# Kernel tuning notes

Hardware: AMD Instinct MI355X
Metric: run time of the kernel (lower is better)

## Reference

```python
import jax, jax.numpy as jnp
import numpy as np

H = 1024  # hidden_dim


def setup_inputs() -> dict:
    key = jax.random.key(0)
    ks = jax.random.split(key, 8)
    B, S = 32, 2048
    value = jax.random.normal(ks[0], (B, S, 2 * H), dtype=jnp.float32)
    query = jax.random.normal(ks[1], (B, 2 * H), dtype=jnp.float32)
    padding_mask = jnp.zeros((B, S), dtype=bool)
    pre_coverage = jax.random.uniform(ks[2], (B, S), dtype=jnp.float32)
    sc = 1.0 / np.sqrt(2 * H)
    Wv = jax.random.normal(ks[3], (2 * H, H), dtype=jnp.float32) * sc  # value_layer.weight^T
    Wq = jax.random.normal(ks[4], (2 * H, H), dtype=jnp.float32) * sc  # query_layer.weight^T
    We = jax.random.normal(ks[5], (H,), dtype=jnp.float32) * (1.0 / np.sqrt(H))  # energy_layer
    Wc = jax.random.normal(ks[6], (H,), dtype=jnp.float32)  # coverage_layer (Linear(1,H))
    return {"value": value, "query": query, "padding_mask": padding_mask,
            "pre_coverage": pre_coverage, "Wv": Wv, "Wq": Wq, "We": We, "Wc": Wc}


def reference(value, query, padding_mask, pre_coverage, Wv, Wq, We, Wc):
    # value: [B,S,2H], query: [B,2H], padding_mask: [B,S] bool, pre_coverage: [B,S]
    v = jnp.einsum('bsf,fh->bsh', value, Wv)          # projected values [B,S,H]
    q = (query @ Wq)[:, None, :]                       # [B,1,H]
    feat = q + v + pre_coverage[:, :, None] * Wc       # coverage term: Linear(1,H)
    scores = jnp.tanh(feat) @ We                       # [B,S]
    scores = jnp.where(padding_mask, -jnp.inf, scores)
    alphas = jax.nn.softmax(scores, axis=-1)           # [B,S]
    context = jnp.einsum('bs,bsh->bh', alphas, v)[:, None, :]  # [B,1,H]
    new_coverage = pre_coverage + alphas
    return context, alphas, new_coverage
```

## Files before the change

kernel.cpp:

```cpp
#include <hip/hip_runtime.h>
#include <hip/hip_bf16.h>

#define HD 1024
#define K2 2048
#define BATCH 32
#define SEQ 2048
#define M_TOT (BATCH * SEQ)

typedef __attribute__((ext_vector_type(4))) float f32x4;
typedef __attribute__((ext_vector_type(8))) short bf16x8;
typedef __attribute__((ext_vector_type(4))) unsigned short u16x4;
typedef __attribute__((ext_vector_type(8))) unsigned short u16x8;
typedef __attribute__((ext_vector_type(4))) unsigned int u32x4;

__device__ __forceinline__ float bf2f(unsigned short u) {
    unsigned int x = ((unsigned int)u) << 16;
    return __builtin_bit_cast(float, x);
}
__device__ __forceinline__ unsigned short f2bf(float f) {
    unsigned int x = __builtin_bit_cast(unsigned int, f);
    unsigned int lsb = (x >> 16) & 1u;
    x += 0x7fffu + lsb;
    return (unsigned short)(x >> 16);
}
__device__ __forceinline__ unsigned int cvt_pk(float lo, float hi) {
    unsigned int r;
    asm("v_cvt_pk_bf16_f32 %0, %1, %2" : "=v"(r) : "v"(lo), "v"(hi));
    return r;
}

__device__ __forceinline__ void load_lds_16B(const void* g, void* lds) {
    __builtin_amdgcn_global_load_lds(
        (const __attribute__((address_space(1))) unsigned int*)g,
        (__attribute__((address_space(3))) unsigned int*)lds,
        16, 0, 0);
}

__global__ __launch_bounds__(256) void wv_transpose_kernel(
        const float* __restrict__ Wv, unsigned short* __restrict__ WvT) {
    __shared__ float t[64][65];
    int n0 = blockIdx.x * 64;
    int k0 = blockIdx.y * 64;
    int tx = threadIdx.x & 63, ty = threadIdx.x >> 6;
#pragma unroll
    for (int rr = 0; rr < 16; ++rr) {
        int row = ty + rr * 4;
        t[row][tx] = Wv[(size_t)(k0 + row) * HD + n0 + tx];
    }
    __syncthreads();
#pragma unroll
    for (int rr = 0; rr < 16; ++rr) {
        int row = ty + rr * 4;
        WvT[(size_t)(n0 + row) * K2 + k0 + tx] = f2bf(t[tx][row]);
    }
}

__global__ __launch_bounds__(256) void qproj_kernel(
        const float* __restrict__ query, const float* __restrict__ Wq,
        float* __restrict__ qp) {
    int b = blockIdx.x >> 2;
    int h = ((blockIdx.x & 3) << 8) + threadIdx.x;
    const float* q = query + (size_t)b * K2;
    float acc = 0.f;
    for (int f = 0; f < K2; f += 4) {
        f32x4 qv = *reinterpret_cast<const f32x4*>(q + f);
        acc += qv.x * Wq[(size_t)f * HD + h];
        acc += qv.y * Wq[(size_t)(f + 1) * HD + h];
        acc += qv.z * Wq[(size_t)(f + 2) * HD + h];
        acc += qv.w * Wq[(size_t)(f + 3) * HD + h];
    }
    qp[b * HD + h] = acc;
}

#define NT 32

__device__ __forceinline__ f32x4 mfma_bf16(bf16x8 a, bf16x8 b, f32x4 c) {
    return __builtin_amdgcn_mfma_f32_16x16x32_bf16(a, b, c, 0, 0, 0);
}

template<int MB, int NB>
__device__ __forceinline__ void mfma_quad(f32x4 (&acc)[8][4],
        const bf16x8 (&af)[4][2], const bf16x8 (&bfv)[2][2]) {
#pragma unroll
    for (int f = 0; f < 4; ++f)
#pragma unroll
        for (int j = 0; j < 2; ++j) {
            acc[MB + f][NB + j] = mfma_bf16(af[f][0], bfv[j][0], acc[MB + f][NB + j]);
            acc[MB + f][NB + j] = mfma_bf16(af[f][1], bfv[j][1], acc[MB + f][NB + j]);
        }
}

__global__ __launch_bounds__(512, 2) void gemm8_kernel(
        const float* __restrict__ A,
        const unsigned short* __restrict__ BT,
        unsigned short* __restrict__ Vout) {
    __shared__ __align__(16) char lds[131072];

    const int tid  = threadIdx.x;
    const int lane = tid & 63;
    const int wave = tid >> 6;
    const int wr   = wave >> 2;
    const int wc   = wave & 3;

    int id  = blockIdx.x;
    int xcd = id & 7, sdx = id >> 3;
    int m0 = ((xcd << 5) | (sdx >> 2)) * 256;
    int n0 = (sdx & 3) * 256;

    const int off0   = wave * 1024 + lane * 16;
    const int srow   = off0 >> 7;
    const int chunk  = (off0 >> 4) & 7;
    const int schunk = chunk ^ (srow & 7);
    const unsigned short* Bs0 = BT + ((size_t)n0 + srow) * K2 + schunk * 8;
    const float* aBase = A + ((size_t)m0 + srow) * K2 + chunk * 8;
    const int woff = srow * 128 + schunk * 16;

    const int l15 = lane & 15, l4v = lane >> 4;
    const int kch0 = (l4v ^ (lane & 7)) << 4;
    const int kch1 = ((4 | l4v) ^ (lane & 7)) << 4;
    const int aRow = (wr * 128 + l15) * 128;
    const int bRow = (wc * 64 + l15) * 128;

    f32x4 acc[8][4] = {};

    f32x4 a0lo, a0hi, a1lo, a1hi, a2lo, a2hi, a3lo, a3hi;

#define LOAD_A(t_) do {                                                       \
        const float* _ap = aBase + (size_t)(t_) * 64;                         \
        a0lo = *(const f32x4*)(_ap);                                          \
        a0hi = *(const f32x4*)(_ap + 4);                                      \
        a1lo = *(const f32x4*)(_ap + (size_t)128 * K2);                       \
        a1hi = *(const f32x4*)(_ap + (size_t)128 * K2 + 4);                   \
        a2lo = *(const f32x4*)(_ap + (size_t)64 * K2);                        \
        a2hi = *(const f32x4*)(_ap + (size_t)64 * K2 + 4);                    \
        a3lo = *(const f32x4*)(_ap + (size_t)192 * K2);                       \
        a3hi = *(const f32x4*)(_ap + (size_t)192 * K2 + 4);                   \
    } while (0)

#define WRITE_A_P0(buf_) do {                                                 \
        u32x4 w0, w1;                                                         \
        w0.x = cvt_pk(a0lo.x, a0lo.y); w0.y = cvt_pk(a0lo.z, a0lo.w);         \
        w0.z = cvt_pk(a0hi.x, a0hi.y); w0.w = cvt_pk(a0hi.z, a0hi.w);         \
        w1.x = cvt_pk(a1lo.x, a1lo.y); w1.y = cvt_pk(a1lo.z, a1lo.w);         \
        w1.z = cvt_pk(a1hi.x, a1hi.y); w1.w = cvt_pk(a1hi.z, a1hi.w);         \
        *reinterpret_cast<u32x4*>(lds + (buf_) * 32768 + 0     + woff) = w0;  \
        *reinterpret_cast<u32x4*>(lds + (buf_) * 32768 + 16384 + woff) = w1;  \
    } while (0)

#define WRITE_A_P1(buf_) do {                                                 \
        u32x4 w2, w3;                                                         \
        w2.x = cvt_pk(a2lo.x, a2lo.y); w2.y = cvt_pk(a2lo.z, a2lo.w);         \
        w2.z = cvt_pk(a2hi.x, a2hi.y); w2.w = cvt_pk(a2hi.z, a2hi.w);         \
        w3.x = cvt_pk(a3lo.x, a3lo.y); w3.y = cvt_pk(a3lo.z, a3lo.w);         \
        w3.z = cvt_pk(a3hi.x, a3hi.y); w3.w = cvt_pk(a3hi.z, a3hi.w);         \
        *reinterpret_cast<u32x4*>(lds + (buf_) * 32768 + 8192  + woff) = w2;  \
        *reinterpret_cast<u32x4*>(lds + (buf_) * 32768 + 24576 + woff) = w3;  \
    } while (0)

#define STG_B(t_, h_, p_, buf_) \
    load_lds_16B(Bs0 + ((size_t)((h_) * 128 + (p_) * 64)) * K2 + (t_) * 64, \
                 lds + 65536 + (buf_) * 32768 + (h_) * 16384 + (p_) * 8192 + off0)

    LOAD_A(0);
    STG_B(0, 0, 0, 0); STG_B(0, 0, 1, 0); STG_B(0, 1, 0, 0); STG_B(0, 1, 1, 0);
    WRITE_A_P0(0); WRITE_A_P1(0);
    LOAD_A(1);
    STG_B(1, 0, 0, 1); STG_B(1, 0, 1, 1); STG_B(1, 1, 0, 1); STG_B(1, 1, 1, 1);
    WRITE_A_P0(1); WRITE_A_P1(1);
    asm volatile("s_waitcnt vmcnt(0) lgkmcnt(0)" ::: "memory");
    __builtin_amdgcn_s_barrier();

    bf16x8 afr[4][2], bf0[2][2], bf1[2][2];

    for (int t = 0; t < NT; ++t) {
        const int cur = t & 1;
        const char* La = lds + cur * 32768;
        const char* Lb = lds + 65536 + cur * 32768;
        const bool pf = (t + 2 < NT);

#pragma unroll
        for (int f = 0; f < 4; ++f) {
            afr[f][0] = *(const bf16x8*)(La + aRow + f * 2048 + kch0);
            afr[f][1] = *(const bf16x8*)(La + aRow + f * 2048 + kch1);
        }
#pragma unroll
        for (int j = 0; j < 2; ++j) {
            bf0[j][0] = *(const bf16x8*)(Lb + bRow + j * 2048 + kch0);
            bf0[j][1] = *(const bf16x8*)(Lb + bRow + j * 2048 + kch1);
        }
        if (pf) LOAD_A(t + 2);
        __builtin_amdgcn_s_barrier();
        asm volatile("s_waitcnt lgkmcnt(0)" ::: "memory");
        __builtin_amdgcn_s_setprio(1);
        mfma_quad<0, 0>(acc, afr, bf0);
        __builtin_amdgcn_s_setprio(0);
        __builtin_amdgcn_s_barrier();

#pragma unroll
        for (int j = 0; j < 2; ++j) {
            bf1[j][0] = *(const bf16x8*)(Lb + bRow + (2 + j) * 2048 + kch0);
            bf1[j][1] = *(const bf16x8*)(Lb + bRow + (2 + j) * 2048 + kch1);
        }
        __builtin_amdgcn_s_barrier();
        asm volatile("s_waitcnt lgkmcnt(0)" ::: "memory");
        __builtin_amdgcn_s_setprio(1);
        mfma_quad<0, 2>(acc, afr, bf1);
        __builtin_amdgcn_s_setprio(0);
        __builtin_amdgcn_s_barrier();

#pragma unroll
        for (int f = 0; f < 4; ++f) {
            afr[f][0] = *(const bf16x8*)(La + aRow + 8192 + f * 2048 + kch0);
            afr[f][1] = *(const bf16x8*)(La + aRow + 8192 + f * 2048 + kch1);
        }
        if (pf) {
            WRITE_A_P0(cur);
            STG_B(t + 2, 0, 0, cur); STG_B(t + 2, 0, 1, cur);
            STG_B(t + 2, 1, 0, cur); STG_B(t + 2, 1, 1, cur);
        }
        __builtin_amdgcn_s_barrier();
        asm volatile("s_waitcnt lgkmcnt(0)" ::: "memory");
        __builtin_amdgcn_s_setprio(1);
        mfma_quad<4, 2>(acc, afr, bf1);
        __builtin_amdgcn_s_setprio(0);
        __builtin_amdgcn_s_barrier();

        if (pf) WRITE_A_P1(cur);
        __builtin_amdgcn_s_barrier();
        asm volatile("s_waitcnt lgkmcnt(0)" ::: "memory");
        __builtin_amdgcn_s_setprio(1);
        mfma_quad<4, 0>(acc, afr, bf0);
        __builtin_amdgcn_s_setprio(0);
        if (t == NT - 2) asm volatile("s_waitcnt vmcnt(0)" ::: "memory");
        if (t < NT - 1) __builtin_amdgcn_s_barrier();
    }
#undef LOAD_A
#undef WRITE_A_P0
#undef WRITE_A_P1
#undef STG_B

#pragma unroll
    for (int fi = 0; fi < 8; ++fi) {
#pragma unroll
        for (int fj = 0; fj < 4; ++fj) {
            int row = m0 + wr * 128 + fi * 16 + l4v * 4;
            int col = n0 + wc * 64 + fj * 16 + l15;
#pragma unroll
            for (int r = 0; r < 4; ++r)
                Vout[(size_t)(row + r) * HD + col] = f2bf(acc[fi][fj][r]);
        }
    }
}

#define BM 128
#define BN 128
#define BK 32
__device__ __forceinline__ void swizzle_mn(int id, int& m0, int& n0) {
    int xcd = id & 7;
    int s = id >> 3;
    int m_idx = (xcd << 6) | (s >> 3);
    int n_idx = s & 7;
    m0 = m_idx * BM;
    n0 = n_idx * BN;
}

__global__ __launch_bounds__(256) void gemm_v_kernel(
        const float* __restrict__ A,
        const unsigned short* __restrict__ BT,
        unsigned short* __restrict__ Vout) {
    __shared__ __align__(16) unsigned short As[BM * BK];
    __shared__ __align__(16) unsigned short Bs[BN * BK];
    const int tid = threadIdx.x;
    const int lane = tid & 63;
    const int wave = tid >> 6;
    const int wr = wave >> 1, wc = wave & 1;
    int m0, n0;
    swizzle_mn(blockIdx.x, m0, n0);
    const int l15 = lane & 15;
    const int l4 = lane >> 4;

    f32x4 acc[4][4] = {};

    for (int kk = 0; kk < K2; kk += BK) {
#pragma unroll
        for (int i = 0; i < 4; ++i) {
            int c = i * 256 + tid;
            int row = c >> 3;
            int col = (c & 7) * 4;
            f32x4 v = *reinterpret_cast<const f32x4*>(
                A + (size_t)(m0 + row) * K2 + kk + col);
            u16x4 bv;
            bv.x = f2bf(v.x); bv.y = f2bf(v.y);
            bv.z = f2bf(v.z); bv.w = f2bf(v.w);
            *reinterpret_cast<u16x4*>(&As[row * BK + col]) = bv;
        }
#pragma unroll
        for (int i = 0; i < 2; ++i) {
            int cb = i * 256 + tid;
            int row = cb >> 2, col = (cb & 3) * 8;
            load_lds_16B(BT + (size_t)(n0 + row) * K2 + kk + col, ((char*)Bs) + cb * 16);
        }
        __syncthreads();

        bf16x8 af[4], bfr[4];
#pragma unroll
        for (int i = 0; i < 4; ++i) {
            int row = wr * 64 + i * 16 + l15;
            af[i] = *reinterpret_cast<const bf16x8*>(&As[row * BK + l4 * 8]);
        }
#pragma unroll
        for (int j = 0; j < 4; ++j) {
            int row = wc * 64 + j * 16 + l15;
            bfr[j] = *reinterpret_cast<const bf16x8*>(&Bs[row * BK + l4 * 8]);
        }
#pragma unroll
        for (int i = 0; i < 4; ++i)
#pragma unroll
            for (int j = 0; j < 4; ++j)
                acc[i][j] = __builtin_amdgcn_mfma_f32_16x16x32_bf16(
                    af[i], bfr[j], acc[i][j], 0, 0, 0);
        __syncthreads();
    }

#pragma unroll
    for (int i = 0; i < 4; ++i) {
#pragma unroll
        for (int j = 0; j < 4; ++j) {
            int row = m0 + wr * 64 + i * 16 + l4 * 4;
            int col = n0 + wc * 64 + j * 16 + l15;
#pragma unroll
            for (int r = 0; r < 4; ++r)
                Vout[(size_t)(row + r) * HD + col] = f2bf(acc[i][j][r]);
        }
    }
}

__global__ __launch_bounds__(256) void score_kernel(
        const unsigned short* __restrict__ V, const float* __restrict__ qp,
        const float* __restrict__ Wc, const float* __restrict__ We,
        const float* __restrict__ pre_cov, float* __restrict__ scores) {
    int lane = threadIdx.x & 63;
    int wave = threadIdx.x >> 6;
    int m = blockIdx.x * 4 + wave;
    int b = m >> 11;
    float pc = pre_cov[m];
    const unsigned short* vp = V + (size_t)m * HD;
    const float* qpb = qp + b * HD;
    float partial = 0.f;
#pragma unroll
    for (int e = 0; e < 16; ++e) {
        int h = e * 64 + lane;
        float f = bf2f(vp[h]) + qpb[h] + pc * Wc[h];
        float t = 1.f - 2.f / (__expf(2.f * f) + 1.f);
        partial += t * We[h];
    }
#pragma unroll
    for (int off = 32; off; off >>= 1)
        partial += __shfl_xor(partial, off);
    if (lane == 0) scores[m] = partial;
}

__global__ __launch_bounds__(256) void softmax_kernel(
        const float* __restrict__ scores, const unsigned char* __restrict__ mask,
        const float* __restrict__ pre_cov, float* __restrict__ out) {
    __shared__ float red[8];
    int b = blockIdx.x;
    int tid = threadIdx.x;
    int lane = tid & 63, wave = tid >> 6;
    float s[8];
#pragma unroll
    for (int i = 0; i < 8; ++i) {
        int idx = b * SEQ + i * 256 + tid;
        float v = scores[idx];
        if (mask[idx]) v = -INFINITY;
        s[i] = v;
    }
    float mx = s[0];
#pragma unroll
    for (int i = 1; i < 8; ++i) mx = fmaxf(mx, s[i]);
#pragma unroll
    for (int off = 32; off; off >>= 1) mx = fmaxf(mx, __shfl_xor(mx, off));
    if (lane == 0) red[wave] = mx;
    __syncthreads();
    mx = fmaxf(fmaxf(red[0], red[1]), fmaxf(red[2], red[3]));

    float e[8]; float sum = 0.f;
#pragma unroll
    for (int i = 0; i < 8; ++i) { e[i] = __expf(s[i] - mx); sum += e[i]; }
#pragma unroll
    for (int off = 32; off; off >>= 1) sum += __shfl_xor(sum, off);
    if (lane == 0) red[4 + wave] = sum;
    __syncthreads();
    sum = red[4] + red[5] + red[6] + red[7];
    float inv = 1.f / sum;
#pragma unroll
    for (int i = 0; i < 8; ++i) {
        int idx = b * SEQ + i * 256 + tid;
        float a = e[i] * inv;
        out[32768 + idx] = a;
        out[32768 + 65536 + idx] = pre_cov[idx] + a;
    }
}

__global__ __launch_bounds__(256) void ctx_part_kernel(
        const unsigned short* __restrict__ V, const float* __restrict__ out,
        float* __restrict__ part) {
    int blk = blockIdx.x;
    int sc = blk & 15;
    int b  = blk >> 4;
    int h4 = threadIdx.x * 4;
    const float* al = out + 32768 + b * SEQ + sc * 128;
    const unsigned short* vp = V + ((size_t)(b * SEQ + sc * 128)) * HD + h4;
    f32x4 acc = {};
#pragma unroll 4
    for (int s = 0; s < 128; ++s) {
        float a = al[s];
        u16x4 v = *reinterpret_cast<const u16x4*>(vp + (size_t)s * HD);
        acc.x += a * bf2f(v.x);
        acc.y += a * bf2f(v.y);
        acc.z += a * bf2f(v.z);
        acc.w += a * bf2f(v.w);
    }
    *reinterpret_cast<f32x4*>(&part[(size_t)(b * 16 + sc) * HD + h4]) = acc;
}

__global__ __launch_bounds__(256) void ctx_reduce_kernel(
        const float* __restrict__ part, float* __restrict__ out) {
    int idx = blockIdx.x * 256 + threadIdx.x;
    int b = idx >> 10, h = idx & 1023;
    float acc = 0.f;
#pragma unroll
    for (int sc = 0; sc < 16; ++sc)
        acc += part[(size_t)(b * 16 + sc) * HD + h];
    out[idx] = acc;
}

extern "C" void kernel_launch(void* const* d_in, const int* in_sizes, int n_in,
                              void* d_out, int out_size, void* d_ws, size_t ws_size,
                              hipStream_t stream) {
    const float* value          = (const float*)d_in[0];
    const float* query          = (const float*)d_in[1];
    const unsigned char* mask   = (const unsigned char*)d_in[2];
    const float* pre_cov        = (const float*)d_in[3];
    const float* Wv             = (const float*)d_in[4];
    const float* Wq             = (const float*)d_in[5];
    const float* We             = (const float*)d_in[6];
    const float* Wc             = (const float*)d_in[7];
    float* out = (float*)d_out;

    char* ws = (char*)d_ws;
    unsigned short* WvT = (unsigned short*)(ws);
    unsigned short* Vbf = (unsigned short*)(ws + ((size_t)4 << 20));
    float* qp           = (float*)(ws + ((size_t)132 << 20));
    float* scores       = (float*)(ws + ((size_t)132 << 20) + (128 << 10));
    float* part         = (float*)(ws + ((size_t)132 << 20) + (384 << 10));

    const bool bigws = ws_size >= ((size_t)136 << 20);

    hipLaunchKernelGGL(wv_transpose_kernel, dim3(16, 32), dim3(256), 0, stream, Wv, WvT);
    hipLaunchKernelGGL(qproj_kernel, dim3(128), dim3(256), 0, stream, query, Wq, qp);
    if (bigws) {
        hipLaunchKernelGGL(gemm8_kernel, dim3(1024), dim3(512), 0, stream, value, WvT, Vbf);
    } else {
        hipLaunchKernelGGL(gemm_v_kernel, dim3(4096), dim3(256), 0, stream, value, WvT, Vbf);
    }
    hipLaunchKernelGGL(score_kernel, dim3(M_TOT / 4), dim3(256), 0, stream,
                       Vbf, qp, Wc, We, pre_cov, scores);
    hipLaunchKernelGGL(softmax_kernel, dim3(BATCH), dim3(256), 0, stream,
                       scores, mask, pre_cov, out);
    hipLaunchKernelGGL(ctx_part_kernel, dim3(512), dim3(256), 0, stream, Vbf, out, part);
    hipLaunchKernelGGL(ctx_reduce_kernel, dim3(128), dim3(256), 0, stream, part, out);
}
```

Baseline: 504.0 us.

## Deepen A-tile global prefetch to three stages with ping-pong register sets

The fp32 A-operand global loads are now issued three K-steps ahead instead of two, using two alternating register sets (setA/setB) and a 2x manually unrolled main loop. The prologue issues the third load and waits only on older vmcnt, so global latency for A has more time to hide behind MFMA work. This doubles the register footprint for staged A data (32 more VGPRs), which under launch_bounds(512,2) risks spills or reduced scheduling freedom. The vmcnt(0) wait at t==NT-2 remains, and the inner loops lost their unroll pragmas inside the macro.

```diff
diff --git a/kernel.cpp b/kernel.cpp
--- a/kernel.cpp
+++ b/kernel.cpp
@@ -90,6 +90,40 @@
         }
 }
 
+struct ASet { f32x4 v0, v1, v2, v3, v4, v5, v6, v7; };
+
+__device__ __forceinline__ void load_a_set(const float* aBase, int t, ASet& s) {
+    const float* ap = aBase + (size_t)t * 64;
+    s.v0 = *(const f32x4*)(ap);
+    s.v1 = *(const f32x4*)(ap + 4);
+    s.v2 = *(const f32x4*)(ap + (size_t)128 * K2);
+    s.v3 = *(const f32x4*)(ap + (size_t)128 * K2 + 4);
+    s.v4 = *(const f32x4*)(ap + (size_t)64 * K2);
+    s.v5 = *(const f32x4*)(ap + (size_t)64 * K2 + 4);
+    s.v6 = *(const f32x4*)(ap + (size_t)192 * K2);
+    s.v7 = *(const f32x4*)(ap + (size_t)192 * K2 + 4);
+}
+
+__device__ __forceinline__ void write_a_p0(char* lds, int buf, int woff, const ASet& s) {
+    u32x4 w0, w1;
+    w0.x = cvt_pk(s.v0.x, s.v0.y); w0.y = cvt_pk(s.v0.z, s.v0.w);
+    w0.z = cvt_pk(s.v1.x, s.v1.y); w0.w = cvt_pk(s.v1.z, s.v1.w);
+    w1.x = cvt_pk(s.v2.x, s.v2.y); w1.y = cvt_pk(s.v2.z, s.v2.w);
+    w1.z = cvt_pk(s.v3.x, s.v3.y); w1.w = cvt_pk(s.v3.z, s.v3.w);
+    *reinterpret_cast<u32x4*>(lds + buf * 32768 + 0     + woff) = w0;
+    *reinterpret_cast<u32x4*>(lds + buf * 32768 + 16384 + woff) = w1;
+}
+
+__device__ __forceinline__ void write_a_p1(char* lds, int buf, int woff, const ASet& s) {
+    u32x4 w2, w3;
+    w2.x = cvt_pk(s.v4.x, s.v4.y); w2.y = cvt_pk(s.v4.z, s.v4.w);
+    w2.z = cvt_pk(s.v5.x, s.v5.y); w2.w = cvt_pk(s.v5.z, s.v5.w);
+    w3.x = cvt_pk(s.v6.x, s.v6.y); w3.y = cvt_pk(s.v6.z, s.v6.w);
+    w3.z = cvt_pk(s.v7.x, s.v7.y); w3.w = cvt_pk(s.v7.z, s.v7.w);
+    *reinterpret_cast<u32x4*>(lds + buf * 32768 + 8192  + woff) = w2;
+    *reinterpret_cast<u32x4*>(lds + buf * 32768 + 24576 + woff) = w3;
+}
+
 __global__ __launch_bounds__(512, 2) void gemm8_kernel(
         const float* __restrict__ A,
         const unsigned short* __restrict__ BT,
@@ -123,120 +157,88 @@
 
     f32x4 acc[8][4] = {};
 
-    f32x4 a0lo, a0hi, a1lo, a1hi, a2lo, a2hi, a3lo, a3hi;
-
-#define LOAD_A(t_) do {                                                       \
-        const float* _ap = aBase + (size_t)(t_) * 64;                         \
-        a0lo = *(const f32x4*)(_ap);                                          \
-        a0hi = *(const f32x4*)(_ap + 4);                                      \
-        a1lo = *(const f32x4*)(_ap + (size_t)128 * K2);                       \
-        a1hi = *(const f32x4*)(_ap + (size_t)128 * K2 + 4);                   \
-        a2lo = *(const f32x4*)(_ap + (size_t)64 * K2);                        \
-        a2hi = *(const f32x4*)(_ap + (size_t)64 * K2 + 4);                    \
-        a3lo = *(const f32x4*)(_ap + (size_t)192 * K2);                       \
-        a3hi = *(const f32x4*)(_ap + (size_t)192 * K2 + 4);                   \
-    } while (0)
-
-#define WRITE_A_P0(buf_) do {                                                 \
-        u32x4 w0, w1;                                                         \
-        w0.x = cvt_pk(a0lo.x, a0lo.y); w0.y = cvt_pk(a0lo.z, a0lo.w);         \
-        w0.z = cvt_pk(a0hi.x, a0hi.y); w0.w = cvt_pk(a0hi.z, a0hi.w);         \
-        w1.x = cvt_pk(a1lo.x, a1lo.y); w1.y = cvt_pk(a1lo.z, a1lo.w);         \
-        w1.z = cvt_pk(a1hi.x, a1hi.y); w1.w = cvt_pk(a1hi.z, a1hi.w);         \
-        *reinterpret_cast<u32x4*>(lds + (buf_) * 32768 + 0     + woff) = w0;  \
-        *reinterpret_cast<u32x4*>(lds + (buf_) * 32768 + 16384 + woff) = w1;  \
-    } while (0)
-
-#define WRITE_A_P1(buf_) do {                                                 \
-        u32x4 w2, w3;                                                         \
-        w2.x = cvt_pk(a2lo.x, a2lo.y); w2.y = cvt_pk(a2lo.z, a2lo.w);         \
-        w2.z = cvt_pk(a2hi.x, a2hi.y); w2.w = cvt_pk(a2hi.z, a2hi.w);         \
-        w3.x = cvt_pk(a3lo.x, a3lo.y); w3.y = cvt_pk(a3lo.z, a3lo.w);         \
-        w3.z = cvt_pk(a3hi.x, a3hi.y); w3.w = cvt_pk(a3hi.z, a3hi.w);         \
-        *reinterpret_cast<u32x4*>(lds + (buf_) * 32768 + 8192  + woff) = w2;  \
-        *reinterpret_cast<u32x4*>(lds + (buf_) * 32768 + 24576 + woff) = w3;  \
-    } while (0)
+    ASet setA, setB;
 
 #define STG_B(t_, h_, p_, buf_) \
     load_lds_16B(Bs0 + ((size_t)((h_) * 128 + (p_) * 64)) * K2 + (t_) * 64, \
                  lds + 65536 + (buf_) * 32768 + (h_) * 16384 + (p_) * 8192 + off0)
 
-    LOAD_A(0);
+    load_a_set(aBase, 0, setA);
     STG_B(0, 0, 0, 0); STG_B(0, 0, 1, 0); STG_B(0, 1, 0, 0); STG_B(0, 1, 1, 0);
-    WRITE_A_P0(0); WRITE_A_P1(0);
-    LOAD_A(1);
+    write_a_p0(lds, 0, woff, setA); write_a_p1(lds, 0, woff, setA);
+    load_a_set(aBase, 1, setA);
     STG_B(1, 0, 0, 1); STG_B(1, 0, 1, 1); STG_B(1, 1, 0, 1); STG_B(1, 1, 1, 1);
-    WRITE_A_P0(1); WRITE_A_P1(1);
-    asm volatile("s_waitcnt vmcnt(0) lgkmcnt(0)" ::: "memory");
+    write_a_p0(lds, 1, woff, setA); write_a_p1(lds, 1, woff, setA);
+    load_a_set(aBase, 2, setA);
+    asm volatile("s_waitcnt vmcnt(8) lgkmcnt(0)" ::: "memory");
     __builtin_amdgcn_s_barrier();
 
     bf16x8 afr[4][2], bf0[2][2], bf1[2][2];
 
-    for (int t = 0; t < NT; ++t) {
-        const int cur = t & 1;
-        const char* La = lds + cur * 32768;
-        const char* Lb = lds + 65536 + cur * 32768;
-        const bool pf = (t + 2 < NT);
-
-#pragma unroll
-        for (int f = 0; f < 4; ++f) {
-            afr[f][0] = *(const bf16x8*)(La + aRow + f * 2048 + kch0);
-            afr[f][1] = *(const bf16x8*)(La + aRow + f * 2048 + kch1);
-        }
-#pragma unroll
-        for (int j = 0; j < 2; ++j) {
-            bf0[j][0] = *(const bf16x8*)(Lb + bRow + j * 2048 + kch0);
-            bf0[j][1] = *(const bf16x8*)(Lb + bRow + j * 2048 + kch1);
-        }
-        if (pf) LOAD_A(t + 2);
-        __builtin_amdgcn_s_barrier();
-        asm volatile("s_waitcnt lgkmcnt(0)" ::: "memory");
-        __builtin_amdgcn_s_setprio(1);
-        mfma_quad<0, 0>(acc, afr, bf0);
-        __builtin_amdgcn_s_setprio(0);
-        __builtin_amdgcn_s_barrier();
-
-#pragma unroll
-        for (int j = 0; j < 2; ++j) {
-            bf1[j][0] = *(const bf16x8*)(Lb + bRow + (2 + j) * 2048 + kch0);
-            bf1[j][1] = *(const bf16x8*)(Lb + bRow + (2 + j) * 2048 + kch1);
-        }
-        __builtin_amdgcn_s_barrier();
-        asm volatile("s_waitcnt lgkmcnt(0)" ::: "memory");
-        __builtin_amdgcn_s_setprio(1);
-        mfma_quad<0, 2>(acc, afr, bf1);
-        __builtin_amdgcn_s_setprio(0);
-        __builtin_amdgcn_s_barrier();
-
-#pragma unroll
-        for (int f = 0; f < 4; ++f) {
-            afr[f][0] = *(const bf16x8*)(La + aRow + 8192 + f * 2048 + kch0);
-            afr[f][1] = *(const bf16x8*)(La + aRow + 8192 + f * 2048 + kch1);
-        }
-        if (pf) {
-            WRITE_A_P0(cur);
-            STG_B(t + 2, 0, 0, cur); STG_B(t + 2, 0, 1, cur);
-            STG_B(t + 2, 1, 0, cur); STG_B(t + 2, 1, 1, cur);
-        }
-        __builtin_amdgcn_s_barrier();
-        asm volatile("s_waitcnt lgkmcnt(0)" ::: "memory");
-        __builtin_amdgcn_s_setprio(1);
-        mfma_quad<4, 2>(acc, afr, bf1);
-        __builtin_amdgcn_s_setprio(0);
-        __builtin_amdgcn_s_barrier();
-
-        if (pf) WRITE_A_P1(cur);
-        __builtin_amdgcn_s_barrier();
-        asm volatile("s_waitcnt lgkmcnt(0)" ::: "memory");
-        __builtin_amdgcn_s_setprio(1);
-        mfma_quad<4, 0>(acc, afr, bf0);
-        __builtin_amdgcn_s_setprio(0);
-        if (t == NT - 2) asm volatile("s_waitcnt vmcnt(0)" ::: "memory");
-        if (t < NT - 1) __builtin_amdgcn_s_barrier();
-    }
-#undef LOAD_A
-#undef WRITE_A_P0
-#undef WRITE_A_P1
+#define ITER(t_, CUR, NXT) do {                                               \
+        const int cur = (t_) & 1;                                             \
+        const char* La = lds + cur * 32768;                                   \
+        const char* Lb = lds + 65536 + cur * 32768;                           \
+        const bool pf = ((t_) + 2 < NT);                                      \
+          \
+        for (int f = 0; f < 4; ++f) {                                         \
+            afr[f][0] = *(const bf16x8*)(La + aRow + f * 2048 + kch0);        \
+            afr[f][1] = *(const bf16x8*)(La + aRow + f * 2048 + kch1);        \
+        }                                                                     \
+        for (int j = 0; j < 2; ++j) {                                         \
+            bf0[j][0] = *(const bf16x8*)(Lb + bRow + j * 2048 + kch0);        \
+            bf0[j][1] = *(const bf16x8*)(Lb + bRow + j * 2048 + kch1);        \
+        }                                                                     \
+        if ((t_) + 3 < NT) load_a_set(aBase, (t_) + 3, NXT);                  \
+        __builtin_amdgcn_s_barrier();                                         \
+        asm volatile("s_waitcnt lgkmcnt(0)" ::: "memory");                    \
+        __builtin_amdgcn_s_setprio(1);                                        \
+        mfma_quad<0, 0>(acc, afr, bf0);                                       \
+        __builtin_amdgcn_s_setprio(0);                                        \
+        __builtin_amdgcn_s_barrier();                                         \
+                                          \
+        for (int j = 0; j < 2; ++j) {                                         \
+            bf1[j][0] = *(const bf16x8*)(Lb + bRow + (2 + j) * 2048 + kch0);  \
+            bf1[j][1] = *(const bf16x8*)(Lb + bRow + (2 + j) * 2048 + kch1);  \
+        }                                                                     \
+        __builtin_amdgcn_s_barrier();                                         \
+        asm volatile("s_waitcnt lgkmcnt(0)" ::: "memory");                    \
+        __builtin_amdgcn_s_setprio(1);                                        \
+        mfma_quad<0, 2>(acc, afr, bf1);                                       \
+        __builtin_amdgcn_s_setprio(0);                                        \
+        __builtin_amdgcn_s_barrier();                                         \
+         \
+        for (int f = 0; f < 4; ++f) {                                         \
+            afr[f][0] = *(const bf16x8*)(La + aRow + 8192 + f * 2048 + kch0); \
+            afr[f][1] = *(const bf16x8*)(La + aRow + 8192 + f * 2048 + kch1); \
+        }                                                                     \
+        if (pf) {                                                             \
+            write_a_p0(lds, cur, woff, CUR);                                  \
+            STG_B((t_) + 2, 0, 0, cur); STG_B((t_) + 2, 0, 1, cur);           \
+            STG_B((t_) + 2, 1, 0, cur); STG_B((t_) + 2, 1, 1, cur);           \
+        }                                                                     \
+        __builtin_amdgcn_s_barrier();                                         \
+        asm volatile("s_waitcnt lgkmcnt(0)" ::: "memory");                    \
+        __builtin_amdgcn_s_setprio(1);                                        \
+        mfma_quad<4, 2>(acc, afr, bf1);                                       \
+        __builtin_amdgcn_s_setprio(0);                                        \
+        __builtin_amdgcn_s_barrier();                                         \
+                         \
+        if (pf) write_a_p1(lds, cur, woff, CUR);                              \
+        __builtin_amdgcn_s_barrier();                                         \
+        asm volatile("s_waitcnt lgkmcnt(0)" ::: "memory");                    \
+        __builtin_amdgcn_s_setprio(1);                                        \
+        mfma_quad<4, 0>(acc, afr, bf0);                                       \
+        __builtin_amdgcn_s_setprio(0);                                        \
+        if ((t_) == NT - 2) asm volatile("s_waitcnt vmcnt(0)" ::: "memory");  \
+        if ((t_) < NT - 1) __builtin_amdgcn_s_barrier();                      \
+    } while (0)
+
+    for (int t = 0; t < NT; t += 2) {
+        ITER(t, setA, setB);
+        ITER(t + 1, setB, setA);
+    }
+#undef ITER
 #undef STG_B
 
 #pragma unroll
```

Result: slower. 939.7 us (+86.5%).

## Replace 256x256 8-wave GEMM with 128x128 4-wave tile kernel

Applied to the files above, without the earlier changes.

Swaps the 256x256-tile, 512-thread value-projection GEMM for a 128x128-tile, 256-thread variant with half the LDS. A-tile global loads, conversion and LDS writes are regrouped into one set per stage, and the first three K-steps are prefetched. The aim is more resident blocks per CU and finer-grained scheduling in exchange for lower per-tile data reuse, so the fp32 A matrix and the B matrix are fetched from global memory more times overall.

```diff
diff --git a/kernel.cpp b/kernel.cpp
--- a/kernel.cpp
+++ b/kernel.cpp
@@ -79,10 +79,10 @@
 }
 
 template<int MB, int NB>
-__device__ __forceinline__ void mfma_quad(f32x4 (&acc)[8][4],
-        const bf16x8 (&af)[4][2], const bf16x8 (&bfv)[2][2]) {
-#pragma unroll
-    for (int f = 0; f < 4; ++f)
+__device__ __forceinline__ void mfma_q4(f32x4 (&acc)[4][4],
+        const bf16x8 (&af)[2][2], const bf16x8 (&bfv)[2][2]) {
+#pragma unroll
+    for (int f = 0; f < 2; ++f)
 #pragma unroll
         for (int j = 0; j < 2; ++j) {
             acc[MB + f][NB + j] = mfma_bf16(af[f][0], bfv[j][0], acc[MB + f][NB + j]);
@@ -90,26 +90,56 @@
         }
 }
 
-__global__ __launch_bounds__(512, 2) void gemm8_kernel(
+struct ASet { f32x4 v0, v1, v2, v3, v4, v5, v6, v7; };
+
+__device__ __forceinline__ void load_a_set(const float* aBase, int t, ASet& s) {
+    const float* ap = aBase + (size_t)t * 64;
+    s.v0 = *(const f32x4*)(ap);
+    s.v1 = *(const f32x4*)(ap + 4);
+    s.v2 = *(const f32x4*)(ap + (size_t)32 * K2);
+    s.v3 = *(const f32x4*)(ap + (size_t)32 * K2 + 4);
+    s.v4 = *(const f32x4*)(ap + (size_t)64 * K2);
+    s.v5 = *(const f32x4*)(ap + (size_t)64 * K2 + 4);
+    s.v6 = *(const f32x4*)(ap + (size_t)96 * K2);
+    s.v7 = *(const f32x4*)(ap + (size_t)96 * K2 + 4);
+}
+
+__device__ __forceinline__ void write_a(char* lds, int buf, int woff, const ASet& s) {
+    u32x4 w0, w1, w2, w3;
+    w0.x = cvt_pk(s.v0.x, s.v0.y); w0.y = cvt_pk(s.v0.z, s.v0.w);
+    w0.z = cvt_pk(s.v1.x, s.v1.y); w0.w = cvt_pk(s.v1.z, s.v1.w);
+    w1.x = cvt_pk(s.v2.x, s.v2.y); w1.y = cvt_pk(s.v2.z, s.v2.w);
+    w1.z = cvt_pk(s.v3.x, s.v3.y); w1.w = cvt_pk(s.v3.z, s.v3.w);
+    w2.x = cvt_pk(s.v4.x, s.v4.y); w2.y = cvt_pk(s.v4.z, s.v4.w);
+    w2.z = cvt_pk(s.v5.x, s.v5.y); w2.w = cvt_pk(s.v5.z, s.v5.w);
+    w3.x = cvt_pk(s.v6.x, s.v6.y); w3.y = cvt_pk(s.v6.z, s.v6.w);
+    w3.z = cvt_pk(s.v7.x, s.v7.y); w3.w = cvt_pk(s.v7.z, s.v7.w);
+    *reinterpret_cast<u32x4*>(lds + buf * 16384 + 0     + woff) = w0;
+    *reinterpret_cast<u32x4*>(lds + buf * 16384 + 4096  + woff) = w1;
+    *reinterpret_cast<u32x4*>(lds + buf * 16384 + 8192  + woff) = w2;
+    *reinterpret_cast<u32x4*>(lds + buf * 16384 + 12288 + woff) = w3;
+}
+
+__global__ __launch_bounds__(256, 2) void gemm128f_kernel(
         const float* __restrict__ A,
         const unsigned short* __restrict__ BT,
         unsigned short* __restrict__ Vout) {
-    __shared__ __align__(16) char lds[131072];
+    __shared__ __align__(16) char lds[65536];
 
     const int tid  = threadIdx.x;
     const int lane = tid & 63;
     const int wave = tid >> 6;
-    const int wr   = wave >> 2;
-    const int wc   = wave & 3;
+    const int wr   = wave >> 1;
+    const int wc   = wave & 1;
 
     int id  = blockIdx.x;
     int xcd = id & 7, sdx = id >> 3;
-    int m0 = ((xcd << 5) | (sdx >> 2)) * 256;
-    int n0 = (sdx & 3) * 256;
-
-    const int off0   = wave * 1024 + lane * 16;
-    const int srow   = off0 >> 7;
-    const int chunk  = (off0 >> 4) & 7;
+    int m0 = ((xcd << 6) | (sdx >> 3)) * 128;
+    int n0 = (sdx & 7) * 128;
+
+    const int off0   = tid * 16;
+    const int srow   = tid >> 3;
+    const int chunk  = tid & 7;
     const int schunk = chunk ^ (srow & 7);
     const unsigned short* Bs0 = BT + ((size_t)n0 + srow) * K2 + schunk * 8;
     const float* aBase = A + ((size_t)m0 + srow) * K2 + chunk * 8;
@@ -118,68 +148,36 @@
     const int l15 = lane & 15, l4v = lane >> 4;
     const int kch0 = (l4v ^ (lane & 7)) << 4;
     const int kch1 = ((4 | l4v) ^ (lane & 7)) << 4;
-    const int aRow = (wr * 128 + l15) * 128;
+    const int aRow = (wr * 64 + l15) * 128;
     const int bRow = (wc * 64 + l15) * 128;
 
-    f32x4 acc[8][4] = {};
-
-    f32x4 a0lo, a0hi, a1lo, a1hi, a2lo, a2hi, a3lo, a3hi;
-
-#define LOAD_A(t_) do {                                                       \
-        const float* _ap = aBase + (size_t)(t_) * 64;                         \
-        a0lo = *(const f32x4*)(_ap);                                          \
-        a0hi = *(const f32x4*)(_ap + 4);                                      \
-        a1lo = *(const f32x4*)(_ap + (size_t)128 * K2);                       \
-        a1hi = *(const f32x4*)(_ap + (size_t)128 * K2 + 4);                   \
-        a2lo = *(const f32x4*)(_ap + (size_t)64 * K2);                        \
-        a2hi = *(const f32x4*)(_ap + (size_t)64 * K2 + 4);                    \
-        a3lo = *(const f32x4*)(_ap + (size_t)192 * K2);                       \
-        a3hi = *(const f32x4*)(_ap + (size_t)192 * K2 + 4);                   \
-    } while (0)
-
-#define WRITE_A_P0(buf_) do {                                                 \
-        u32x4 w0, w1;                                                         \
-        w0.x = cvt_pk(a0lo.x, a0lo.y); w0.y = cvt_pk(a0lo.z, a0lo.w);         \
-        w0.z = cvt_pk(a0hi.x, a0hi.y); w0.w = cvt_pk(a0hi.z, a0hi.w);         \
-        w1.x = cvt_pk(a1lo.x, a1lo.y); w1.y = cvt_pk(a1lo.z, a1lo.w);         \
-        w1.z = cvt_pk(a1hi.x, a1hi.y); w1.w = cvt_pk(a1hi.z, a1hi.w);         \
-        *reinterpret_cast<u32x4*>(lds + (buf_) * 32768 + 0     + woff) = w0;  \
-        *reinterpret_cast<u32x4*>(lds + (buf_) * 32768 + 16384 + woff) = w1;  \
-    } while (0)
-
-#define WRITE_A_P1(buf_) do {                                                 \
-        u32x4 w2, w3;                                                         \
-        w2.x = cvt_pk(a2lo.x, a2lo.y); w2.y = cvt_pk(a2lo.z, a2lo.w);         \
-        w2.z = cvt_pk(a2hi.x, a2hi.y); w2.w = cvt_pk(a2hi.z, a2hi.w);         \
-        w3.x = cvt_pk(a3lo.x, a3lo.y); w3.y = cvt_pk(a3lo.z, a3lo.w);         \
-        w3.z = cvt_pk(a3hi.x, a3hi.y); w3.w = cvt_pk(a3hi.z, a3hi.w);         \
-        *reinterpret_cast<u32x4*>(lds + (buf_) * 32768 + 8192  + woff) = w2;  \
-        *reinterpret_cast<u32x4*>(lds + (buf_) * 32768 + 24576 + woff) = w3;  \
-    } while (0)
-
-#define STG_B(t_, h_, p_, buf_) \
-    load_lds_16B(Bs0 + ((size_t)((h_) * 128 + (p_) * 64)) * K2 + (t_) * 64, \
-                 lds + 65536 + (buf_) * 32768 + (h_) * 16384 + (p_) * 8192 + off0)
-
-    LOAD_A(0);
-    STG_B(0, 0, 0, 0); STG_B(0, 0, 1, 0); STG_B(0, 1, 0, 0); STG_B(0, 1, 1, 0);
-    WRITE_A_P0(0); WRITE_A_P1(0);
-    LOAD_A(1);
-    STG_B(1, 0, 0, 1); STG_B(1, 0, 1, 1); STG_B(1, 1, 0, 1); STG_B(1, 1, 1, 1);
-    WRITE_A_P0(1); WRITE_A_P1(1);
-    asm volatile("s_waitcnt vmcnt(0) lgkmcnt(0)" ::: "memory");
+    f32x4 acc[4][4] = {};
+    ASet s;
+
+#define STG_B(t_, p_, buf_) \
+    load_lds_16B(Bs0 + ((size_t)(32 * (p_))) * K2 + (t_) * 64, \
+                 lds + 32768 + (buf_) * 16384 + (p_) * 4096 + off0)
+
+    load_a_set(aBase, 0, s);
+    STG_B(0, 0, 0); STG_B(0, 1, 0); STG_B(0, 2, 0); STG_B(0, 3, 0);
+    write_a(lds, 0, woff, s);
+    load_a_set(aBase, 1, s);
+    STG_B(1, 0, 1); STG_B(1, 1, 1); STG_B(1, 2, 1); STG_B(1, 3, 1);
+    write_a(lds, 1, woff, s);
+    load_a_set(aBase, 2, s);
+    asm volatile("s_waitcnt lgkmcnt(0)" ::: "memory");
     __builtin_amdgcn_s_barrier();
 
-    bf16x8 afr[4][2], bf0[2][2], bf1[2][2];
+    bf16x8 afr[2][2], bf0[2][2], bf1[2][2];
 
     for (int t = 0; t < NT; ++t) {
         const int cur = t & 1;
-        const char* La = lds + cur * 32768;
-        const char* Lb = lds + 65536 + cur * 32768;
+        const char* La = lds + cur * 16384;
+        const char* Lb = lds + 32768 + cur * 16384;
         const bool pf = (t + 2 < NT);
 
 #pragma unroll
-        for (int f = 0; f < 4; ++f) {
+        for (int f = 0; f < 2; ++f) {
             afr[f][0] = *(const bf16x8*)(La + aRow + f * 2048 + kch0);
             afr[f][1] = *(const bf16x8*)(La + aRow + f * 2048 + kch1);
         }
@@ -188,11 +186,11 @@
             bf0[j][0] = *(const bf16x8*)(Lb + bRow + j * 2048 + kch0);
             bf0[j][1] = *(const bf16x8*)(Lb + bRow + j * 2048 + kch1);
         }
-        if (pf) LOAD_A(t + 2);
+        if (pf) load_a_set(aBase, t + 2, s);
         __builtin_amdgcn_s_barrier();
         asm volatile("s_waitcnt lgkmcnt(0)" ::: "memory");
         __builtin_amdgcn_s_setprio(1);
-        mfma_quad<0, 0>(acc, afr, bf0);
+        mfma_q4<0, 0>(acc, afr, bf0);
         __builtin_amdgcn_s_setprio(0);
         __builtin_amdgcn_s_barrier();
 
@@ -204,46 +202,40 @@
         __builtin_amdgcn_s_barrier();
         asm volatile("s_waitcnt lgkmcnt(0)" ::: "memory");
         __builtin_amdgcn_s_setprio(1);
-        mfma_quad<0, 2>(acc, afr, bf1);
+        mfma_q4<0, 2>(acc, afr, bf1);
         __builtin_amdgcn_s_setprio(0);
         __builtin_amdgcn_s_barrier();
 
 #pragma unroll
-        for (int f = 0; f < 4; ++f) {
-            afr[f][0] = *(const bf16x8*)(La + aRow + 8192 + f * 2048 + kch0);
-            afr[f][1] = *(const bf16x8*)(La + aRow + 8192 + f * 2048 + kch1);
-        }
-        if (pf) {
-            WRITE_A_P0(cur);
-            STG_B(t + 2, 0, 0, cur); STG_B(t + 2, 0, 1, cur);
-            STG_B(t + 2, 1, 0, cur); STG_B(t + 2, 1, 1, cur);
-        }
+        for (int f = 0; f < 2; ++f) {
+            afr[f][0] = *(const bf16x8*)(La + aRow + 4096 + f * 2048 + kch0);
+            afr[f][1] = *(const bf16x8*)(La + aRow + 4096 + f * 2048 + kch1);
+        }
+        if (pf) { STG_B(t + 2, 0, cur); STG_B(t + 2, 1, cur);
+                  STG_B(t + 2, 2, cur); STG_B(t + 2, 3, cur); }
         __builtin_amdgcn_s_barrier();
         asm volatile("s_waitcnt lgkmcnt(0)" ::: "memory");
         __builtin_amdgcn_s_setprio(1);
-        mfma_quad<4, 2>(acc, afr, bf1);
+        mfma_q4<2, 2>(acc, afr, bf1);
         __builtin_amdgcn_s_setprio(0);
         __builtin_amdgcn_s_barrier();
 
-        if (pf) WRITE_A_P1(cur);
+        if (pf) write_a(lds, cur, woff, s);
         __builtin_amdgcn_s_barrier();
         asm volatile("s_waitcnt lgkmcnt(0)" ::: "memory");
         __builtin_amdgcn_s_setprio(1);
-        mfma_quad<4, 0>(acc, afr, bf0);
+        mfma_q4<2, 0>(acc, afr, bf0);
         __builtin_amdgcn_s_setprio(0);
         if (t == NT - 2) asm volatile("s_waitcnt vmcnt(0)" ::: "memory");
         if (t < NT - 1) __builtin_amdgcn_s_barrier();
     }
-#undef LOAD_A
-#undef WRITE_A_P0
-#undef WRITE_A_P1
 #undef STG_B
 
 #pragma unroll
-    for (int fi = 0; fi < 8; ++fi) {
+    for (int fi = 0; fi < 4; ++fi) {
 #pragma unroll
         for (int fj = 0; fj < 4; ++fj) {
-            int row = m0 + wr * 128 + fi * 16 + l4v * 4;
+            int row = m0 + wr * 64 + fi * 16 + l4v * 4;
             int col = n0 + wc * 64 + fj * 16 + l15;
 #pragma unroll
             for (int r = 0; r < 4; ++r)
@@ -460,7 +452,7 @@
     hipLaunchKernelGGL(wv_transpose_kernel, dim3(16, 32), dim3(256), 0, stream, Wv, WvT);
     hipLaunchKernelGGL(qproj_kernel, dim3(128), dim3(256), 0, stream, query, Wq, qp);
     if (bigws) {
-        hipLaunchKernelGGL(gemm8_kernel, dim3(1024), dim3(512), 0, stream, value, WvT, Vbf);
+        hipLaunchKernelGGL(gemm128f_kernel, dim3(4096), dim3(256), 0, stream, value, WvT, Vbf);
     } else {
         hipLaunchKernelGGL(gemm_v_kernel, dim3(4096), dim3(256), 0, stream, value, WvT, Vbf);
     }
```

Measured after the change: 590.0 us. +17.1%, slower.

## Fuse tanh-energy score computation into GEMM epilogue with partial-score reduction

Applied to the files above, without the earlier changes.

Computes the tanh(q+v+cov*Wc)·We score contributions directly from the fp32 GEMM accumulators in the gemm8 epilogue. Each wave writes a per-row partial over its 64 columns into a 16-wide partial buffer, and a new softmax kernel sums those partials. This removes the separate score kernel, which re-read the full bf16 V matrix. It adds epilogue ALU work, shuffles and extra partial-score traffic, and needs a larger workspace threshold for the fast path.

```diff
diff --git a/kernel.cpp b/kernel.cpp
--- a/kernel.cpp
+++ b/kernel.cpp
@@ -93,7 +93,12 @@
 __global__ __launch_bounds__(512, 2) void gemm8_kernel(
         const float* __restrict__ A,
         const unsigned short* __restrict__ BT,
-        unsigned short* __restrict__ Vout) {
+        unsigned short* __restrict__ Vout,
+        const float* __restrict__ qp,
+        const float* __restrict__ Wc,
+        const float* __restrict__ We,
+        const float* __restrict__ pre_cov,
+        float* __restrict__ scores_part) {
     __shared__ __align__(16) char lds[131072];
 
     const int tid  = threadIdx.x;
@@ -137,36 +142,40 @@
         a3hi = *(const f32x4*)(_ap + (size_t)192 * K2 + 4);                   \
     } while (0)
 
-#define WRITE_A_P0(buf_) do {                                                 \
+#define WRITE_A_P0() do {                                                     \
         u32x4 w0, w1;                                                         \
         w0.x = cvt_pk(a0lo.x, a0lo.y); w0.y = cvt_pk(a0lo.z, a0lo.w);         \
         w0.z = cvt_pk(a0hi.x, a0hi.y); w0.w = cvt_pk(a0hi.z, a0hi.w);         \
         w1.x = cvt_pk(a1lo.x, a1lo.y); w1.y = cvt_pk(a1lo.z, a1lo.w);         \
         w1.z = cvt_pk(a1hi.x, a1hi.y); w1.w = cvt_pk(a1hi.z, a1hi.w);         \
-        *reinterpret_cast<u32x4*>(lds + (buf_) * 32768 + 0     + woff) = w0;  \
-        *reinterpret_cast<u32x4*>(lds + (buf_) * 32768 + 16384 + woff) = w1;  \
+        *reinterpret_cast<u32x4*>(lds + _buf * 32768 + 0     + woff) = w0;    \
+        *reinterpret_cast<u32x4*>(lds + _buf * 32768 + 16384 + woff) = w1;    \
     } while (0)
 
-#define WRITE_A_P1(buf_) do {                                                 \
+#define WRITE_A_P1() do {                                                     \
         u32x4 w2, w3;                                                         \
         w2.x = cvt_pk(a2lo.x, a2lo.y); w2.y = cvt_pk(a2lo.z, a2lo.w);         \
         w2.z = cvt_pk(a2hi.x, a2hi.y); w2.w = cvt_pk(a2hi.z, a2hi.w);         \
         w3.x = cvt_pk(a3lo.x, a3lo.y); w3.y = cvt_pk(a3lo.z, a3lo.w);         \
         w3.z = cvt_pk(a3hi.x, a3hi.y); w3.w = cvt_pk(a3hi.z, a3hi.w);         \
-        *reinterpret_cast<u32x4*>(lds + (buf_) * 32768 + 8192  + woff) = w2;  \
-        *reinterpret_cast<u32x4*>(lds + (buf_) * 32768 + 24576 + woff) = w3;  \
+        *reinterpret_cast<u32x4*>(lds + _buf * 32768 + 8192  + woff) = w2;    \
+        *reinterpret_cast<u32x4*>(lds + _buf * 32768 + 24576 + woff) = w3;    \
     } while (0)
 
 #define STG_B(t_, h_, p_, buf_) \
     load_lds_16B(Bs0 + ((size_t)((h_) * 128 + (p_) * 64)) * K2 + (t_) * 64, \
                  lds + 65536 + (buf_) * 32768 + (h_) * 16384 + (p_) * 8192 + off0)
 
-    LOAD_A(0);
-    STG_B(0, 0, 0, 0); STG_B(0, 0, 1, 0); STG_B(0, 1, 0, 0); STG_B(0, 1, 1, 0);
-    WRITE_A_P0(0); WRITE_A_P1(0);
-    LOAD_A(1);
-    STG_B(1, 0, 0, 1); STG_B(1, 0, 1, 1); STG_B(1, 1, 0, 1); STG_B(1, 1, 1, 1);
-    WRITE_A_P0(1); WRITE_A_P1(1);
+    {
+        int _buf = 0;
+        LOAD_A(0);
+        STG_B(0, 0, 0, 0); STG_B(0, 0, 1, 0); STG_B(0, 1, 0, 0); STG_B(0, 1, 1, 0);
+        WRITE_A_P0(); WRITE_A_P1();
+        _buf = 1;
+        LOAD_A(1);
+        STG_B(1, 0, 0, 1); STG_B(1, 0, 1, 1); STG_B(1, 1, 0, 1); STG_B(1, 1, 1, 1);
+        WRITE_A_P0(); WRITE_A_P1();
+    }
     asm volatile("s_waitcnt vmcnt(0) lgkmcnt(0)" ::: "memory");
     __builtin_amdgcn_s_barrier();
 
@@ -174,6 +183,7 @@
 
     for (int t = 0; t < NT; ++t) {
         const int cur = t & 1;
+        const int _buf = cur;
         const char* La = lds + cur * 32768;
         const char* Lb = lds + 65536 + cur * 32768;
         const bool pf = (t + 2 < NT);
@@ -214,7 +224,7 @@
             afr[f][1] = *(const bf16x8*)(La + aRow + 8192 + f * 2048 + kch1);
         }
         if (pf) {
-            WRITE_A_P0(cur);
+            WRITE_A_P0();
             STG_B(t + 2, 0, 0, cur); STG_B(t + 2, 0, 1, cur);
             STG_B(t + 2, 1, 0, cur); STG_B(t + 2, 1, 1, cur);
         }
@@ -225,7 +235,7 @@
         __builtin_amdgcn_s_setprio(0);
         __builtin_amdgcn_s_barrier();
 
-        if (pf) WRITE_A_P1(cur);
+        if (pf) WRITE_A_P1();
         __builtin_amdgcn_s_barrier();
         asm volatile("s_waitcnt lgkmcnt(0)" ::: "memory");
         __builtin_amdgcn_s_setprio(1);
@@ -238,6 +248,39 @@
 #undef WRITE_A_P0
 #undef WRITE_A_P1
 #undef STG_B
+
+    {
+        const int b = m0 >> 11;
+        const int nb = n0 >> 8;
+        float qpv[4], wcv[4], wev[4];
+#pragma unroll
+        for (int fj = 0; fj < 4; ++fj) {
+            int col = n0 + wc * 64 + fj * 16 + l15;
+            qpv[fj] = qp[b * HD + col];
+            wcv[fj] = Wc[col];
+            wev[fj] = We[col];
+        }
+#pragma unroll
+        for (int fi = 0; fi < 8; ++fi) {
+#pragma unroll
+            for (int r = 0; r < 4; ++r) {
+                int row = m0 + wr * 128 + fi * 16 + l4v * 4 + r;
+                float pc = pre_cov[row];
+                float partial = 0.f;
+#pragma unroll
+                for (int fj = 0; fj < 4; ++fj) {
+                    float x = acc[fi][fj][r] + qpv[fj] + pc * wcv[fj];
+                    float th = 1.f - 2.f / (__expf(2.f * x) + 1.f);
+                    partial += th * wev[fj];
+                }
+#pragma unroll
+                for (int off = 1; off < 16; off <<= 1)
+                    partial += __shfl_xor(partial, off);
+                if (l15 == 0)
+                    scores_part[(size_t)row * 16 + nb * 4 + wc] = partial;
+            }
+        }
+    }
 
 #pragma unroll
     for (int fi = 0; fi < 8; ++fi) {
@@ -358,6 +401,54 @@
     for (int off = 32; off; off >>= 1)
         partial += __shfl_xor(partial, off);
     if (lane == 0) scores[m] = partial;
+}
+
+__global__ __launch_bounds__(256) void softmax_sp_kernel(
+        const float* __restrict__ sp, const unsigned char* __restrict__ mask,
+        const float* __restrict__ pre_cov, float* __restrict__ out) {
+    __shared__ float red[8];
+    int b = blockIdx.x;
+    int tid = threadIdx.x;
+    int lane = tid & 63, wave = tid >> 6;
+    float s[8];
+#pragma unroll
+    for (int i = 0; i < 8; ++i) {
+        int idx = b * SEQ + i * 256 + tid;
+        const float* p = sp + (size_t)idx * 16;
+        f32x4 p0 = *(const f32x4*)(p);
+        f32x4 p1 = *(const f32x4*)(p + 4);
+        f32x4 p2 = *(const f32x4*)(p + 8);
+        f32x4 p3 = *(const f32x4*)(p + 12);
+        float v = ((p0.x + p0.y) + (p0.z + p0.w)) + ((p1.x + p1.y) + (p1.z + p1.w))
+                + ((p2.x + p2.y) + (p2.z + p2.w)) + ((p3.x + p3.y) + (p3.z + p3.w));
+        if (mask[idx]) v = -INFINITY;
+        s[i] = v;
+    }
+    float mx = s[0];
+#pragma unroll
+    for (int i = 1; i < 8; ++i) mx = fmaxf(mx, s[i]);
+#pragma unroll
+    for (int off = 32; off; off >>= 1) mx = fmaxf(mx, __shfl_xor(mx, off));
+    if (lane == 0) red[wave] = mx;
+    __syncthreads();
+    mx = fmaxf(fmaxf(red[0], red[1]), fmaxf(red[2], red[3]));
+
+    float e[8]; float sum = 0.f;
+#pragma unroll
+    for (int i = 0; i < 8; ++i) { e[i] = __expf(s[i] - mx); sum += e[i]; }
+#pragma unroll
+    for (int off = 32; off; off >>= 1) sum += __shfl_xor(sum, off);
+    if (lane == 0) red[4 + wave] = sum;
+    __syncthreads();
+    sum = red[4] + red[5] + red[6] + red[7];
+    float inv = 1.f / sum;
+#pragma unroll
+    for (int i = 0; i < 8; ++i) {
+        int idx = b * SEQ + i * 256 + tid;
+        float a = e[i] * inv;
+        out[32768 + idx] = a;
+        out[32768 + 65536 + idx] = pre_cov[idx] + a;
+    }
 }
 
 __global__ __launch_bounds__(256) void softmax_kernel(
@@ -452,22 +543,25 @@
     unsigned short* WvT = (unsigned short*)(ws);
     unsigned short* Vbf = (unsigned short*)(ws + ((size_t)4 << 20));
     float* qp           = (float*)(ws + ((size_t)132 << 20));
-    float* scores       = (float*)(ws + ((size_t)132 << 20) + (128 << 10));
-    float* part         = (float*)(ws + ((size_t)132 << 20) + (384 << 10));
-
-    const bool bigws = ws_size >= ((size_t)136 << 20);
+    float* scores_part  = (float*)(ws + ((size_t)132 << 20) + (128 << 10));
+    float* part         = (float*)(ws + ((size_t)137 << 20));
+
+    const bool bigws = ws_size >= ((size_t)140 << 20);
 
     hipLaunchKernelGGL(wv_transpose_kernel, dim3(16, 32), dim3(256), 0, stream, Wv, WvT);
     hipLaunchKernelGGL(qproj_kernel, dim3(128), dim3(256), 0, stream, query, Wq, qp);
     if (bigws) {
-        hipLaunchKernelGGL(gemm8_kernel, dim3(1024), dim3(512), 0, stream, value, WvT, Vbf);
+        hipLaunchKernelGGL(gemm8_kernel, dim3(1024), dim3(512), 0, stream,
+                           value, WvT, Vbf, qp, Wc, We, pre_cov, scores_part);
+        hipLaunchKernelGGL(softmax_sp_kernel, dim3(BATCH), dim3(256), 0, stream,
+                           scores_part, mask, pre_cov, out);
     } else {
         hipLaunchKernelGGL(gemm_v_kernel, dim3(4096), dim3(256), 0, stream, value, WvT, Vbf);
-    }
-    hipLaunchKernelGGL(score_kernel, dim3(M_TOT / 4), dim3(256), 0, stream,
-                       Vbf, qp, Wc, We, pre_cov, scores);
-    hipLaunchKernelGGL(softmax_kernel, dim3(BATCH), dim3(256), 0, stream,
-                       scores, mask, pre_cov, out);
+        hipLaunchKernelGGL(score_kernel, dim3(M_TOT / 4), dim3(256), 0, stream,
+                           Vbf, qp, Wc, We, pre_cov, scores_part);
+        hipLaunchKernelGGL(softmax_kernel, dim3(BATCH), dim3(256), 0, stream,
+                           scores_part, mask, pre_cov, out);
+    }
     hipLaunchKernelGGL(ctx_part_kernel, dim3(512), dim3(256), 0, stream, Vbf, out, part);
     hipLaunchKernelGGL(ctx_reduce_kernel, dim3(128), dim3(256), 0, stream, part, out);
 }
```

Result: slower. 520.7 us (+3.3%).
